# Optimization experiments

Measured on AMD Instinct MI355X. Metric: run time of the kernel, lower is better.

The kernel has to match this reference:

```python
import jax, jax.numpy as jnp
import numpy as np

NUM_HEADS = 16
TEMPERATURE = 1.0


def setup_inputs() -> dict:
    key = jax.random.key(0)
    ks = jax.random.split(key, 6)
    B, H = 2048, 2048
    return {
        "hidden_states": jax.random.normal(ks[0], (B, H), dtype=jnp.float32),
        "attention_mask": jnp.ones((B,), dtype=bool),
        "Wq": jax.random.normal(ks[1], (H, H), dtype=jnp.float32) * 0.02,
        "Wk": jax.random.normal(ks[2], (H, H), dtype=jnp.float32) * 0.02,
        "Wv": jax.random.normal(ks[3], (H, H), dtype=jnp.float32) * 0.02,
        "Wo": jax.random.normal(ks[4], (H, H), dtype=jnp.float32) * 0.02,
        "scale_param": jnp.full((1,), -3.0, dtype=jnp.float32),
    }


def reference(hidden_states, attention_mask, Wq, Wk, Wv, Wo, scale_param):
    B, H = hidden_states.shape
    nh = NUM_HEADS
    hd = H // nh
    # projections (torch Linear: x @ W.T), reshape to [heads, batch, head_dim]
    q = (hidden_states @ Wq.T).reshape(B, nh, hd).transpose(1, 0, 2)
    k = (hidden_states @ Wk.T).reshape(B, nh, hd).transpose(1, 0, 2)
    v = (hidden_states @ Wv.T).reshape(B, nh, hd).transpose(1, 0, 2)
    # cross-batch scores [heads, B, B]
    scores = jnp.einsum('hqd,hkd->hqk', q, k) / (hd ** 0.5 * TEMPERATURE)
    neg_inf = jnp.float32(-jnp.inf)
    eye = jnp.eye(B, dtype=bool)  # exclude self-attention (diagonal)
    scores = jnp.where(eye[None, :, :], neg_inf, scores)
    scores = jnp.where(attention_mask[None, None, :], scores, neg_inf)
    attn = jax.nn.softmax(scores, axis=-1)
    attn = jnp.nan_to_num(attn, nan=0.0)  # rows fully masked -> 0 (dropout=0 is identity)
    ctx = jnp.einsum('hqk,hkd->hqd', attn, v)  # [heads, B, head_dim]
    ctx = ctx.transpose(1, 0, 2).reshape(B, H)
    cross = ctx @ Wo.T
    scale = jax.nn.sigmoid(scale_param[0])
    return hidden_states + scale * cross
```

## Files before the change

### kernel.cpp

```cpp
#include <hip/hip_runtime.h>

typedef __bf16 bf16;
typedef __attribute__((ext_vector_type(8))) __bf16 bf16x8;
typedef __attribute__((ext_vector_type(4))) float f32x4;
typedef __attribute__((ext_vector_type(4))) short s16x4;

#define HDIM 2048

__device__ __forceinline__ void glds16(const void* g, void* l) {
  __builtin_amdgcn_global_load_lds((const __attribute__((address_space(1))) void*)g,
                                   (__attribute__((address_space(3))) void*)l,
                                   16, 0, 0);
}

#define MFMA16(a, b, c) __builtin_amdgcn_mfma_f32_16x16x32_bf16(a, b, c, 0, 0, 0)

__global__ __launch_bounds__(256) void cvt5(
    const float* __restrict__ s0, const float* __restrict__ s1,
    const float* __restrict__ s2, const float* __restrict__ s3,
    const float* __restrict__ s4,
    bf16* __restrict__ d0, bf16* __restrict__ d1, bf16* __restrict__ d2,
    bf16* __restrict__ d3, bf16* __restrict__ d4) {
  const float* s; bf16* d;
  switch (blockIdx.y) {
    case 0: s = s0; d = d0; break;
    case 1: s = s1; d = d1; break;
    case 2: s = s2; d = d2; break;
    case 3: s = s3; d = d3; break;
    default: s = s4; d = d4; break;
  }
  const size_t base = (size_t)blockIdx.x * 4096 + (threadIdx.x << 2);
  for (int i = 0; i < 4; i++) {
    const float4 v = *(const float4*)(s + base + i * 1024);
    union { bf16 h[4]; s16x4 s4v; } u;
    u.h[0] = (bf16)v.x; u.h[1] = (bf16)v.y; u.h[2] = (bf16)v.z; u.h[3] = (bf16)v.w;
    *(s16x4*)(d + base + i * 1024) = u.s4v;
  }
}

__device__ __forceinline__ void gemm128_core(const bf16* __restrict__ A,
                                             const bf16* __restrict__ B,
                                             int rowBase, int colBase,
                                             f32x4 acc[4][4],
                                             bf16* ldsA, bf16* ldsB) {
  const int t = threadIdx.x;
  const int w = t >> 6, l = t & 63;

  for (int mi = 0; mi < 4; mi++)
    for (int ni = 0; ni < 4; ni++)
      for (int r = 0; r < 4; r++) acc[mi][ni][r] = 0.f;

  const int fr = l & 15;
  const int fc = (l >> 4) << 3;
  const bf16* gA0 = A + (size_t)(rowBase + w * 32 + fr) * HDIM + fc;
  const bf16* gA1 = gA0 + (size_t)16 * HDIM;
  const bf16* gB0 = B + (size_t)(colBase + w * 32 + fr) * HDIM + fc;
  const bf16* gB1 = gB0 + (size_t)16 * HDIM;
  bf16* lA = ldsA + (w << 10);
  bf16* lB = ldsB + (w << 10);

  const int af0 = (w >> 1) << 2;
  const int bf0 = (w & 1) << 2;

  for (int k0 = 0; k0 < HDIM; k0 += 32) {
    glds16(gA0, lA);
    glds16(gA1, lA + 512);
    glds16(gB0, lB);
    glds16(gB1, lB + 512);
    gA0 += 32; gA1 += 32; gB0 += 32; gB1 += 32;
    __syncthreads();

    bf16x8 af[4], bfr[4];
    for (int mi = 0; mi < 4; mi++)
      af[mi] = *(const bf16x8*)&ldsA[(af0 + mi) * 512 + l * 8];
    for (int ni = 0; ni < 4; ni++)
      bfr[ni] = *(const bf16x8*)&ldsB[(bf0 + ni) * 512 + l * 8];
    for (int mi = 0; mi < 4; mi++)
      for (int ni = 0; ni < 4; ni++)
        acc[mi][ni] = MFMA16(af[mi], bfr[ni], acc[mi][ni]);
    __syncthreads();
  }
}

__global__ __launch_bounds__(256) void qkv_gemm(
    const bf16* __restrict__ hs, const bf16* __restrict__ Wq,
    const bf16* __restrict__ Wk, const bf16* __restrict__ Wv,
    bf16* __restrict__ qb, bf16* __restrict__ Kf, bf16* __restrict__ Vf) {
  __shared__ bf16 ldsA[128 * 32];
  __shared__ bf16 ldsB[128 * 32];
  const int z = blockIdx.z;
  const bf16* W = (z == 0) ? Wq : (z == 1) ? Wk : Wv;
  const int rowBase = blockIdx.y << 7, colBase = blockIdx.x << 7;
  f32x4 acc[4][4];
  gemm128_core(hs, W, rowBase, colBase, acc, ldsA, ldsB);

  const int t = threadIdx.x;
  const int w = t >> 6, l = t & 63;
  const int wr = (w >> 1) << 6, wc = (w & 1) << 6;
  const int lr = l & 15, lq = l >> 4;

  if (z == 0) {
    for (int mi = 0; mi < 4; mi++)
      for (int ni = 0; ni < 4; ni++) {
        const int col = colBase + wc + ni * 16 + lr;
        const int row0 = rowBase + wr + mi * 16 + lq * 4;
        for (int r = 0; r < 4; r++)
          qb[(size_t)(row0 + r) * HDIM + col] = (bf16)acc[mi][ni][r];
      }
  } else if (z == 1) {
    for (int mi = 0; mi < 4; mi++)
      for (int ni = 0; ni < 4; ni++) {
        const int dim = colBase + wc + ni * 16 + lr;
        const int hh = dim >> 7, ks = (dim >> 5) & 3, kh = (dim >> 3) & 3, j = dim & 7;
        const int row0 = rowBase + wr + mi * 16 + lq * 4;
        for (int r = 0; r < 4; r++) {
          const int key = row0 + r;
          const int kbk = key >> 7, kni = (key >> 4) & 7, kl = key & 15;
          Kf[(((size_t)hh * 16 + kbk) * 32 + kni * 4 + ks) * 512 +
             (kh * 16 + kl) * 8 + j] = (bf16)acc[mi][ni][r];
        }
      }
  } else {
    for (int mi = 0; mi < 4; mi++)
      for (int ni = 0; ni < 4; ni++) {
        const int dim = colBase + wc + ni * 16 + lr;
        const int hh = dim >> 7, vni = (dim >> 4) & 7, ll = dim & 15;
        const int row0 = rowBase + wr + mi * 16 + lq * 4;
        const int kbk = row0 >> 7, ks = (row0 >> 5) & 3, lh = (row0 >> 3) & 3;
        const int j0 = row0 & 7;
        union { bf16 h4[4]; s16x4 v; } u;
        for (int r = 0; r < 4; r++) u.h4[r] = (bf16)acc[mi][ni][r];
        *(s16x4*)&Vf[(((size_t)hh * 16 + kbk) * 32 + vni * 4 + ks) * 512 +
                     (lh * 16 + ll) * 8 + j0] = u.v;
      }
  }
}

__global__ __launch_bounds__(256, 2) void attn_kernel(
    const bf16* __restrict__ qb, const bf16* __restrict__ Kf,
    const bf16* __restrict__ Vf, const unsigned char* __restrict__ amask,
    bf16* __restrict__ ctx) {
  __shared__ bf16 Kl[32 * 512];
  __shared__ bf16 Vl[32 * 512];
  __shared__ bf16 Pl[4 * 2048];

  const int qt = blockIdx.x, h = blockIdx.y;
  const int t = threadIdx.x, w = t >> 6, l = t & 63;
  const int lr = l & 15, lq = l >> 4;
  const int wq = w & 1, wk = w >> 1;
  bf16* Pw = Pl + (w << 11);

  bf16x8 aq[2][4];
  for (int mi = 0; mi < 2; mi++)
    for (int ks = 0; ks < 4; ks++)
      aq[mi][ks] = *(const bf16x8*)&qb[(size_t)(qt * 64 + wq * 32 + mi * 16 + lr) * HDIM +
                                       h * 128 + ks * 32 + lq * 8];

  f32x4 o[2][8];
  for (int mi = 0; mi < 2; mi++)
    for (int ni = 0; ni < 8; ni++)
      for (int r = 0; r < 4; r++) o[mi][ni][r] = 0.f;
  float lsum[2] = {0.f, 0.f};

  const float c = 0.08838834764831845f * 1.4426950408889634f;
  const int lr7 = lr & 7;

  for (int kbk = 0; kbk < 16; kbk++) {
    const size_t tileOff = ((size_t)h * 16 + kbk) * 32 * 512;

    for (int i = 0; i < 8; i++) {
      const int frag = i * 4 + w;
      glds16(Kf + tileOff + frag * 512 + l * 8, Kl + frag * 512);
    }
    bf16x8 vtmp[8];
    for (int i = 0; i < 8; i++)
      vtmp[i] = *(const bf16x8*)&Vf[tileOff + (i * 4 + w) * 512 + l * 8];
    for (int i = 0; i < 8; i++)
      *(bf16x8*)&Vl[(i * 4 + w) * 512 + l * 8] = vtmp[i];
    __syncthreads();

    f32x4 s[2][4];
    for (int mi = 0; mi < 2; mi++)
      for (int ni = 0; ni < 4; ni++)
        for (int r = 0; r < 4; r++) s[mi][ni][r] = 0.f;
    for (int ks = 0; ks < 4; ks++) {
      bf16x8 bk[4];
      for (int ni = 0; ni < 4; ni++)
        bk[ni] = *(const bf16x8*)&Kl[((wk * 4 + ni) * 4 + ks) * 512 + l * 8];
      for (int mi = 0; mi < 2; mi++)
        for (int ni = 0; ni < 4; ni++)
          s[mi][ni] = MFMA16(bk[ni], aq[mi][ks], s[mi][ni]);
    }

    const bool dblk = (((kbk << 1) | wk) == qt);
    for (int ni = 0; ni < 4; ni++) {
      const int kbase = kbk * 128 + wk * 64 + ni * 16 + lq * 4;
      const unsigned mword = *(const unsigned*)&amask[kbase];
      for (int mi = 0; mi < 2; mi++) {
        const int qrowg = qt * 64 + wq * 32 + mi * 16 + lr;
        for (int r = 0; r < 4; r++) {
          float p = __builtin_exp2f(s[mi][ni][r] * c);
          if (!((mword >> (8 * r)) & 0xffu)) p = 0.f;
          if (dblk && (kbase + r == qrowg)) p = 0.f;
          s[mi][ni][r] = p;
          lsum[mi] += p;
        }
      }
    }

    for (int mi = 0; mi < 2; mi++)
      for (int ni = 0; ni < 4; ni++) {
        union { bf16 h4[4]; s16x4 v; } u;
        for (int r = 0; r < 4; r++) u.h4[r] = (bf16)s[mi][ni][r];
        const int row = mi * 16 + lr;
        const int g = ((ni * 2 + (lq >> 1)) ^ lr7);
        *(s16x4*)&Pw[row * 64 + (g << 3) + ((lq & 1) << 2)] = u.v;
      }

    for (int ks2 = 0; ks2 < 2; ks2++) {
      bf16x8 ap[2];
      for (int mi = 0; mi < 2; mi++)
        ap[mi] = *(const bf16x8*)&Pw[(mi * 16 + lr) * 64 +
                                     (((ks2 * 4 + lq) ^ lr7) << 3)];
      for (int ni = 0; ni < 8; ni++) {
        const bf16x8 bv = *(const bf16x8*)&Vl[(ni * 4 + wk * 2 + ks2) * 512 + l * 8];
        for (int mi = 0; mi < 2; mi++)
          o[mi][ni] = MFMA16(ap[mi], bv, o[mi][ni]);
      }
    }
    __syncthreads();
  }

  for (int mi = 0; mi < 2; mi++) {
    lsum[mi] += __shfl_xor(lsum[mi], 16);
    lsum[mi] += __shfl_xor(lsum[mi], 32);
  }

  float* Ocomb = (float*)Kl;
  float* Ls = (float*)Vl;
  if (wk == 1) {
    f32x4* dst = (f32x4*)Ocomb + wq * 1024;
    for (int i = 0; i < 16; i++) dst[i * 64 + l] = o[i >> 3][i & 7];
    if (lq == 0) {
      Ls[wq * 32 + lr] = lsum[0];
      Ls[wq * 32 + 16 + lr] = lsum[1];
    }
  }
  __syncthreads();
  if (wk == 0) {
    const f32x4* src = (const f32x4*)Ocomb + wq * 1024;
    for (int i = 0; i < 16; i++) {
      const f32x4 v = src[i * 64 + l];
      for (int r = 0; r < 4; r++) o[i >> 3][i & 7][r] += v[r];
    }
    lsum[0] += Ls[wq * 32 + lr];
    lsum[1] += Ls[wq * 32 + 16 + lr];
    Ls[64 + wq * 32 + lr] = lsum[0];
    Ls[64 + wq * 32 + 16 + lr] = lsum[1];
  }
  __syncthreads();
  if (wk == 0) {
    for (int mi = 0; mi < 2; mi++)
      for (int r = 0; r < 4; r++) {
        const float li = Ls[64 + wq * 32 + mi * 16 + lq * 4 + r];
        const int row = qt * 64 + wq * 32 + mi * 16 + lq * 4 + r;
        for (int ni = 0; ni < 8; ni++) {
          const float val = (li > 0.f) ? o[mi][ni][r] / li : 0.f;
          ctx[(size_t)row * HDIM + h * 128 + ni * 16 + lr] = (bf16)val;
        }
      }
  }
}

__global__ __launch_bounds__(256) void out_gemm(
    const bf16* __restrict__ ctx, const bf16* __restrict__ Wo,
    const float* __restrict__ hs, const float* __restrict__ scale_p,
    float* __restrict__ outp) {
  __shared__ bf16 ldsA[128 * 32];
  __shared__ bf16 ldsB[64 * 32];
  const int rowBase = blockIdx.y << 7, colBase = blockIdx.x << 6;
  const int t = threadIdx.x;
  const int w = t >> 6, l = t & 63;
  const int wr = (w >> 1) << 6, wc = (w & 1) << 5;
  const int lr = l & 15, lq = l >> 4;

  f32x4 acc[4][2];
  for (int mi = 0; mi < 4; mi++)
    for (int ni = 0; ni < 2; ni++)
      for (int r = 0; r < 4; r++) acc[mi][ni][r] = 0.f;

  const int fr = l & 15;
  const int fc = (l >> 4) << 3;
  const bf16* gA0 = ctx + (size_t)(rowBase + w * 32 + fr) * HDIM + fc;
  const bf16* gA1 = gA0 + (size_t)16 * HDIM;
  const bf16* gB0 = Wo + (size_t)(colBase + w * 16 + fr) * HDIM + fc;
  bf16* lA = ldsA + (w << 10);
  bf16* lB = ldsB + (w << 9);

  const int af0 = (w >> 1) << 2;
  const int bf0 = (w & 1) << 1;

  for (int k0 = 0; k0 < HDIM; k0 += 32) {
    glds16(gA0, lA);
    glds16(gA1, lA + 512);
    glds16(gB0, lB);
    gA0 += 32; gA1 += 32; gB0 += 32;
    __syncthreads();

    bf16x8 af[4], bfr[2];
    for (int mi = 0; mi < 4; mi++)
      af[mi] = *(const bf16x8*)&ldsA[(af0 + mi) * 512 + l * 8];
    for (int ni = 0; ni < 2; ni++)
      bfr[ni] = *(const bf16x8*)&ldsB[(bf0 + ni) * 512 + l * 8];
    for (int mi = 0; mi < 4; mi++)
      for (int ni = 0; ni < 2; ni++)
        acc[mi][ni] = MFMA16(af[mi], bfr[ni], acc[mi][ni]);
    __syncthreads();
  }

  const float sig = 1.0f / (1.0f + __expf(-scale_p[0]));
  for (int mi = 0; mi < 4; mi++)
    for (int ni = 0; ni < 2; ni++) {
      const int col = colBase + wc + ni * 16 + lr;
      const int row0 = rowBase + wr + mi * 16 + lq * 4;
      for (int r = 0; r < 4; r++) {
        const size_t idx = (size_t)(row0 + r) * HDIM + col;
        outp[idx] = hs[idx] + sig * acc[mi][ni][r];
      }
    }
}

extern "C" void kernel_launch(void* const* d_in, const int* in_sizes, int n_in,
                              void* d_out, int out_size, void* d_ws, size_t ws_size,
                              hipStream_t stream) {
  const float* hs = (const float*)d_in[0];
  const unsigned char* amask = (const unsigned char*)d_in[1];
  const float* Wq = (const float*)d_in[2];
  const float* Wk = (const float*)d_in[3];
  const float* Wv = (const float*)d_in[4];
  const float* Wo = (const float*)d_in[5];
  const float* scale_p = (const float*)d_in[6];
  float* outp = (float*)d_out;

  const size_t N = (size_t)HDIM * HDIM;
  bf16* qb   = (bf16*)d_ws;
  bf16* Kf   = qb + N;
  bf16* Vf   = Kf + N;
  bf16* ctx  = Vf + N;
  bf16* hs16 = ctx + N;
  bf16* Wq16 = hs16 + N;
  bf16* Wk16 = Wq16 + N;
  bf16* Wv16 = Wk16 + N;
  bf16* Wo16 = Wv16 + N;

  cvt5<<<dim3(1024, 5), 256, 0, stream>>>(hs, Wq, Wk, Wv, Wo,
                                          hs16, Wq16, Wk16, Wv16, Wo16);
  qkv_gemm<<<dim3(16, 16, 3), 256, 0, stream>>>(hs16, Wq16, Wk16, Wv16, qb, Kf, Vf);
  attn_kernel<<<dim3(32, 16), 256, 0, stream>>>(qb, Kf, Vf, amask, ctx);
  out_gemm<<<dim3(32, 16), 256, 0, stream>>>(ctx, Wo16, hs, scale_p, outp);
}
```

Measured before the change: 323.5 us.

## Double-buffer GEMM LDS tiles with register prefetch and padded row layout

Replaces the direct global-to-LDS loads in the QKV and output projection GEMMs with register-staged loads of the next K tile, issued before the current tile's MFMAs and written into the alternate LDS buffer afterwards. This leaves one barrier per iteration instead of two and hides global latency behind compute. The LDS tiles move from a fragment-packed layout to a row-major layout padded to 36 elements per row to limit bank conflicts. The cost is double the LDS footprint plus extra VGPRs for the staged data, which may lower occupancy, and explicit ds_write instructions now replace the direct-to-LDS path.

```diff
diff --git a/kernel.cpp b/kernel.cpp
--- a/kernel.cpp
+++ b/kernel.cpp
@@ -6,6 +6,7 @@
 typedef __attribute__((ext_vector_type(4))) short s16x4;
 
 #define HDIM 2048
+#define LDST 36
 
 __device__ __forceinline__ void glds16(const void* g, void* l) {
   __builtin_amdgcn_global_load_lds((const __attribute__((address_space(1))) void*)g,
@@ -38,47 +39,60 @@
   }
 }
 
-__device__ __forceinline__ void gemm128_core(const bf16* __restrict__ A,
-                                             const bf16* __restrict__ B,
-                                             int rowBase, int colBase,
-                                             f32x4 acc[4][4],
-                                             bf16* ldsA, bf16* ldsB) {
-  const int t = threadIdx.x;
-  const int w = t >> 6, l = t & 63;
+__device__ __forceinline__ void gemm128_db(const bf16* __restrict__ A,
+                                           const bf16* __restrict__ B,
+                                           int rowBase, int colBase,
+                                           f32x4 acc[4][4],
+                                           bf16* ldsA, bf16* ldsB) {
+  const int t = threadIdx.x, w = t >> 6, l = t & 63;
+  const int wr = (w >> 1) << 6, wc = (w & 1) << 6;
+  const int lr = l & 15, lq = l >> 4;
+  const int sr = l >> 2, sc = (l & 3) << 3;
+  const int BUF = 128 * LDST;
+
+  const bf16* gA0 = A + (size_t)(rowBase + w * 32 + sr) * HDIM + sc;
+  const bf16* gA1 = gA0 + (size_t)16 * HDIM;
+  const bf16* gB0 = B + (size_t)(colBase + w * 32 + sr) * HDIM + sc;
+  const bf16* gB1 = gB0 + (size_t)16 * HDIM;
+  const int wo0 = (w * 32 + sr) * LDST + sc;
+  const int wo1 = wo0 + 16 * LDST;
 
   for (int mi = 0; mi < 4; mi++)
     for (int ni = 0; ni < 4; ni++)
       for (int r = 0; r < 4; r++) acc[mi][ni][r] = 0.f;
 
-  const int fr = l & 15;
-  const int fc = (l >> 4) << 3;
-  const bf16* gA0 = A + (size_t)(rowBase + w * 32 + fr) * HDIM + fc;
-  const bf16* gA1 = gA0 + (size_t)16 * HDIM;
-  const bf16* gB0 = B + (size_t)(colBase + w * 32 + fr) * HDIM + fc;
-  const bf16* gB1 = gB0 + (size_t)16 * HDIM;
-  bf16* lA = ldsA + (w << 10);
-  bf16* lB = ldsB + (w << 10);
-
-  const int af0 = (w >> 1) << 2;
-  const int bf0 = (w & 1) << 2;
-
-  for (int k0 = 0; k0 < HDIM; k0 += 32) {
-    glds16(gA0, lA);
-    glds16(gA1, lA + 512);
-    glds16(gB0, lB);
-    glds16(gB1, lB + 512);
-    gA0 += 32; gA1 += 32; gB0 += 32; gB1 += 32;
-    __syncthreads();
-
+  bf16x8 ra0 = *(const bf16x8*)gA0, ra1 = *(const bf16x8*)gA1;
+  bf16x8 rb0 = *(const bf16x8*)gB0, rb1 = *(const bf16x8*)gB1;
+  gA0 += 32; gA1 += 32; gB0 += 32; gB1 += 32;
+  *(bf16x8*)&ldsA[wo0] = ra0; *(bf16x8*)&ldsA[wo1] = ra1;
+  *(bf16x8*)&ldsB[wo0] = rb0; *(bf16x8*)&ldsB[wo1] = rb1;
+  __syncthreads();
+
+  int p = 0;
+  for (int k = 0; k < 64; k++) {
+    if (k < 63) {
+      ra0 = *(const bf16x8*)gA0; ra1 = *(const bf16x8*)gA1;
+      rb0 = *(const bf16x8*)gB0; rb1 = *(const bf16x8*)gB1;
+      gA0 += 32; gA1 += 32; gB0 += 32; gB1 += 32;
+    }
+    const bf16* bufA = ldsA + p * BUF;
+    const bf16* bufB = ldsB + p * BUF;
     bf16x8 af[4], bfr[4];
     for (int mi = 0; mi < 4; mi++)
-      af[mi] = *(const bf16x8*)&ldsA[(af0 + mi) * 512 + l * 8];
+      af[mi] = *(const bf16x8*)&bufA[(wr + mi * 16 + lr) * LDST + lq * 8];
     for (int ni = 0; ni < 4; ni++)
-      bfr[ni] = *(const bf16x8*)&ldsB[(bf0 + ni) * 512 + l * 8];
+      bfr[ni] = *(const bf16x8*)&bufB[(wc + ni * 16 + lr) * LDST + lq * 8];
     for (int mi = 0; mi < 4; mi++)
       for (int ni = 0; ni < 4; ni++)
         acc[mi][ni] = MFMA16(af[mi], bfr[ni], acc[mi][ni]);
+    if (k < 63) {
+      bf16* dA = ldsA + (p ^ 1) * BUF;
+      bf16* dB = ldsB + (p ^ 1) * BUF;
+      *(bf16x8*)&dA[wo0] = ra0; *(bf16x8*)&dA[wo1] = ra1;
+      *(bf16x8*)&dB[wo0] = rb0; *(bf16x8*)&dB[wo1] = rb1;
+    }
     __syncthreads();
+    p ^= 1;
   }
 }
 
@@ -86,13 +100,13 @@
     const bf16* __restrict__ hs, const bf16* __restrict__ Wq,
     const bf16* __restrict__ Wk, const bf16* __restrict__ Wv,
     bf16* __restrict__ qb, bf16* __restrict__ Kf, bf16* __restrict__ Vf) {
-  __shared__ bf16 ldsA[128 * 32];
-  __shared__ bf16 ldsB[128 * 32];
+  __shared__ bf16 ldsA[2 * 128 * LDST];
+  __shared__ bf16 ldsB[2 * 128 * LDST];
   const int z = blockIdx.z;
   const bf16* W = (z == 0) ? Wq : (z == 1) ? Wk : Wv;
   const int rowBase = blockIdx.y << 7, colBase = blockIdx.x << 7;
   f32x4 acc[4][4];
-  gemm128_core(hs, W, rowBase, colBase, acc, ldsA, ldsB);
+  gemm128_db(hs, W, rowBase, colBase, acc, ldsA, ldsB);
 
   const int t = threadIdx.x;
   const int w = t >> 6, l = t & 63;
@@ -276,46 +290,59 @@
     const bf16* __restrict__ ctx, const bf16* __restrict__ Wo,
     const float* __restrict__ hs, const float* __restrict__ scale_p,
     float* __restrict__ outp) {
-  __shared__ bf16 ldsA[128 * 32];
-  __shared__ bf16 ldsB[64 * 32];
+  __shared__ bf16 ldsA[2 * 128 * LDST];
+  __shared__ bf16 ldsB[2 * 64 * LDST];
   const int rowBase = blockIdx.y << 7, colBase = blockIdx.x << 6;
-  const int t = threadIdx.x;
-  const int w = t >> 6, l = t & 63;
+  const int t = threadIdx.x, w = t >> 6, l = t & 63;
   const int wr = (w >> 1) << 6, wc = (w & 1) << 5;
   const int lr = l & 15, lq = l >> 4;
+  const int sr = l >> 2, sc = (l & 3) << 3;
+  const int BUFA = 128 * LDST, BUFB = 64 * LDST;
+
+  const bf16* gA0 = ctx + (size_t)(rowBase + w * 32 + sr) * HDIM + sc;
+  const bf16* gA1 = gA0 + (size_t)16 * HDIM;
+  const bf16* gB0 = Wo + (size_t)(colBase + w * 16 + sr) * HDIM + sc;
+  const int woA0 = (w * 32 + sr) * LDST + sc;
+  const int woA1 = woA0 + 16 * LDST;
+  const int woB = (w * 16 + sr) * LDST + sc;
 
   f32x4 acc[4][2];
   for (int mi = 0; mi < 4; mi++)
     for (int ni = 0; ni < 2; ni++)
       for (int r = 0; r < 4; r++) acc[mi][ni][r] = 0.f;
 
-  const int fr = l & 15;
-  const int fc = (l >> 4) << 3;
-  const bf16* gA0 = ctx + (size_t)(rowBase + w * 32 + fr) * HDIM + fc;
-  const bf16* gA1 = gA0 + (size_t)16 * HDIM;
-  const bf16* gB0 = Wo + (size_t)(colBase + w * 16 + fr) * HDIM + fc;
-  bf16* lA = ldsA + (w << 10);
-  bf16* lB = ldsB + (w << 9);
-
-  const int af0 = (w >> 1) << 2;
-  const int bf0 = (w & 1) << 1;
-
-  for (int k0 = 0; k0 < HDIM; k0 += 32) {
-    glds16(gA0, lA);
-    glds16(gA1, lA + 512);
-    glds16(gB0, lB);
-    gA0 += 32; gA1 += 32; gB0 += 32;
-    __syncthreads();
-
+  bf16x8 ra0 = *(const bf16x8*)gA0, ra1 = *(const bf16x8*)gA1;
+  bf16x8 rb0 = *(const bf16x8*)gB0;
+  gA0 += 32; gA1 += 32; gB0 += 32;
+  *(bf16x8*)&ldsA[woA0] = ra0; *(bf16x8*)&ldsA[woA1] = ra1;
+  *(bf16x8*)&ldsB[woB] = rb0;
+  __syncthreads();
+
+  int p = 0;
+  for (int k = 0; k < 64; k++) {
+    if (k < 63) {
+      ra0 = *(const bf16x8*)gA0; ra1 = *(const bf16x8*)gA1;
+      rb0 = *(const bf16x8*)gB0;
+      gA0 += 32; gA1 += 32; gB0 += 32;
+    }
+    const bf16* bufA = ldsA + p * BUFA;
+    const bf16* bufB = ldsB + p * BUFB;
     bf16x8 af[4], bfr[2];
     for (int mi = 0; mi < 4; mi++)
-      af[mi] = *(const bf16x8*)&ldsA[(af0 + mi) * 512 + l * 8];
+      af[mi] = *(const bf16x8*)&bufA[(wr + mi * 16 + lr) * LDST + lq * 8];
     for (int ni = 0; ni < 2; ni++)
-      bfr[ni] = *(const bf16x8*)&ldsB[(bf0 + ni) * 512 + l * 8];
+      bfr[ni] = *(const bf16x8*)&bufB[(wc + ni * 16 + lr) * LDST + lq * 8];
     for (int mi = 0; mi < 4; mi++)
       for (int ni = 0; ni < 2; ni++)
         acc[mi][ni] = MFMA16(af[mi], bfr[ni], acc[mi][ni]);
+    if (k < 63) {
+      bf16* dA = ldsA + (p ^ 1) * BUFA;
+      bf16* dB = ldsB + (p ^ 1) * BUFB;
+      *(bf16x8*)&dA[woA0] = ra0; *(bf16x8*)&dA[woA1] = ra1;
+      *(bf16x8*)&dB[woB] = rb0;
+    }
     __syncthreads();
+    p ^= 1;
   }
 
   const float sig = 1.0f / (1.0f + __expf(-scale_p[0]));
```

Result: slower. 567.1 us (+75.3%).
